# Kernel optimization log

Measured on AMD Instinct MI355X. Metric: run time of the kernel, lower is better.

## Reference

```python
import jax, jax.numpy as jnp
import numpy as np

EMBED = 1024
HEADS = 16
HEAD_DIM = EMBED // HEADS


def setup_inputs() -> dict:
    key = jax.random.key(0)
    ks = jax.random.split(key, 6)
    N, S = 4, 1024
    query = jax.random.normal(ks[0], (N, S, EMBED), dtype=jnp.float32)
    keys = jax.random.normal(ks[1], (N, S, EMBED), dtype=jnp.float32)
    values = jax.random.normal(ks[2], (N, S, EMBED), dtype=jnp.float32)
    mask = jax.random.randint(ks[3], (N, 1, S, S), 0, 2, dtype=jnp.int32)
    W_out = jax.random.normal(ks[4], (EMBED, EMBED), dtype=jnp.float32) * (1.0 / np.sqrt(EMBED))
    b_out = jax.random.normal(ks[5], (EMBED,), dtype=jnp.float32) * 0.02
    return {"query": query, "keys": keys, "values": values, "mask": mask,
            "W_out": W_out, "b_out": b_out}


def reference(query, keys, values, mask, W_out, b_out):
    N, Q, _ = query.shape
    K = keys.shape[1]
    # NOTE: the torch module never applies its per-head q/k/v Linear layers;
    # only the reshape + attention + fc_out are in the forward path.
    q = query.reshape(N, Q, HEADS, HEAD_DIM)
    k = keys.reshape(N, K, HEADS, HEAD_DIM)
    v = values.reshape(N, K, HEADS, HEAD_DIM)
    # energy: [N, H, Q, K]
    energy = jnp.einsum("bqhd,bkhd->bhqk", q, k)
    energy = jnp.where(mask == 0, jnp.float32(-1e20), energy)
    attn = jax.nn.softmax(energy / jnp.sqrt(jnp.float32(HEAD_DIM)), axis=3)
    out = jnp.einsum("bhqk,bkhd->bqhd", attn, v).reshape(N, Q, HEADS * HEAD_DIM)
    return out @ W_out.T + b_out
```

## Files before the change

kernel.cpp:

```cpp
#include <hip/hip_runtime.h>
#include <math.h>

#define NB 4
#define SL 1024
#define EMB 1024
#define NH 16
#define HD 64
#define QB 128

typedef __attribute__((ext_vector_type(8))) short bf16x8;
typedef __attribute__((ext_vector_type(4))) float f32x4;

static __device__ __forceinline__ unsigned pk2(float a, float b) {
    unsigned x = __float_as_uint(a) + 0x8000u;
    unsigned y = __float_as_uint(b) + 0x8000u;
    return (x >> 16) | (y & 0xFFFF0000u);
}
static __device__ __forceinline__ float exp2_fast(float x) {
    float r; asm("v_exp_f32 %0, %1" : "=v"(r) : "v"(x)); return r;
}
static __device__ __forceinline__ void gload_lds16(const void* g, void* l) {
    __builtin_amdgcn_global_load_lds(
        (const __attribute__((address_space(1))) unsigned int*)g,
        (__attribute__((address_space(3))) unsigned int*)l, 16, 0, 0);
}

#define VMW(n) asm volatile("s_waitcnt vmcnt(" #n ")" ::: "memory")
#define MEMPIN() asm volatile("" ::: "memory")

__global__ __launch_bounds__(256) void prep(
    const float* __restrict__ W, unsigned short* __restrict__ Wb,
    const float* __restrict__ Kf, unsigned short* __restrict__ Kb,
    const float* __restrict__ V, unsigned short* __restrict__ Vt,
    const int* __restrict__ mask, unsigned long long* __restrict__ Mbt)
{
    __shared__ unsigned short sT[128 * 68];
    const int bid = blockIdx.x, tid = threadIdx.x;

    if (bid < 512) {
        int i = (bid * 256 + tid) * 8;
        float4 f0 = *(const float4*)&W[i];
        float4 f1 = *(const float4*)&W[i + 4];
        uint4 u = { pk2(f0.x,f0.y), pk2(f0.z,f0.w), pk2(f1.x,f1.y), pk2(f1.z,f1.w) };
        *(uint4*)&Wb[i] = u;
    } else if (bid < 2560) {
        int t = bid - 512;
        int b = t >> 9, h = (t >> 5) & 15, k0 = (t & 31) * 32;
        int r = tid >> 3, d = (tid & 7) * 8;
        const float* gp = &Kf[((size_t)(b * SL + k0 + r)) * EMB + h * HD + d];
        float4 f0 = *(const float4*)gp, f1 = *(const float4*)(gp + 4);
        uint4 u = { pk2(f0.x,f0.y), pk2(f0.z,f0.w), pk2(f1.x,f1.y), pk2(f1.z,f1.w) };
        *(uint4*)&Kb[((size_t)((b * NH + h) * SL + k0 + r)) * HD + d] = u;
    } else if (bid < 3072) {
        int t = bid - 2560;
        int bh = t >> 3, kb = t & 7;
        int b = bh >> 4, h = bh & 15;
        int k0 = kb * 128;
        #pragma unroll
        for (int i = 0; i < 4; ++i) {
            int lin = (i * 256 + tid) * 8;
            int r = lin >> 6, d = lin & 63;
            const float* gp = &V[((size_t)(b * SL + k0 + r)) * EMB + h * HD + d];
            float4 f0 = *(const float4*)gp, f1 = *(const float4*)(gp + 4);
            uint2 u0 = { pk2(f0.x,f0.y), pk2(f0.z,f0.w) };
            uint2 u1 = { pk2(f1.x,f1.y), pk2(f1.z,f1.w) };
            *(uint2*)&sT[r * 68 + d]     = u0;
            *(uint2*)&sT[r * 68 + d + 4] = u1;
        }
        __syncthreads();
        #pragma unroll
        for (int p = 0; p < 4; ++p) {
            int d = p * 16 + (tid >> 4);
            int c = tid & 15;
            unsigned v[4];
            #pragma unroll
            for (int j = 0; j < 4; ++j) {
                unsigned lo = sT[(c * 8 + 2 * j) * 68 + d];
                unsigned hi = sT[(c * 8 + 2 * j + 1) * 68 + d];
                v[j] = lo | (hi << 16);
            }
            uint4 u = { v[0], v[1], v[2], v[3] };
            *(uint4*)&Vt[((size_t)(bh * HD + d)) * SL + k0 + c * 8] = u;
        }
    } else {
        int t = bid - 3072;
        int lane = tid & 63;
        #pragma unroll
        for (int r = 0; r < 4; ++r) {
            int wid = (t * 4 + (tid >> 6)) * 4 + r;
            int c = wid & 15, q = (wid >> 4) & 1023, bb = wid >> 14;
            int mv = mask[((size_t)bb * SL + q) * SL + c * 64 + lane];
            unsigned long long bits = __ballot(mv != 0);
            if (lane == 0) Mbt[((size_t)bb * 16 + c) * SL + q] = bits;
        }
    }
}

__global__ __launch_bounds__(256, 2) void attn_mfma(
    const float* __restrict__ Q, const unsigned short* __restrict__ Kb,
    const unsigned short* __restrict__ Vt,
    const unsigned long long* __restrict__ Mbt,
    unsigned short* __restrict__ Oa)
{
    const int lin = blockIdx.x;
    const int xcd = lin & 7, slot = lin >> 3;
    const int bh = xcd * 8 + (slot >> 3);
    const int q0 = (slot & 7) * QB;
    const int b = bh >> 4, h = bh & 15;
    const int tid = threadIdx.x;
    const int w = tid >> 6, lane = tid & 63;
    const int m16 = lane & 15, quad = lane >> 4;
    const int lr = lane >> 3, lc = lane & 7;
    const int sr0 = tid >> 3;

    __shared__ __align__(16) unsigned short sK[3][64 * 64];
    __shared__ __align__(16) unsigned short sVt[3][64 * 64];
    __shared__ __align__(16) unsigned short sPQ[QB * 72];
    __shared__ uint2 lut[16];

    if (tid < 16) {
        unsigned w0 = ((tid & 1) ? 0xFFFFu : 0u) | ((tid & 2) ? 0xFFFF0000u : 0u);
        unsigned w1 = ((tid & 4) ? 0xFFFFu : 0u) | ((tid & 8) ? 0xFFFF0000u : 0u);
        lut[tid] = make_uint2(w0, w1);
    }

    const size_t vbase = (size_t)(bh * HD) * SL;
    const size_t kbase = (size_t)(bh * SL) * HD;
    const size_t mbase = (size_t)(b * 16) * SL + q0 + w * 32 + m16;

    float4 qf[4][2];
    #pragma unroll
    for (int it = 0; it < 4; ++it) {
        int r = sr0 + it * 32;
        const float* gp = &Q[((size_t)(b * SL + q0 + r)) * EMB + h * HD + lc * 8];
        qf[it][0] = *(const float4*)gp;
        qf[it][1] = *(const float4*)(gp + 4);
    }
    MEMPIN();
    unsigned long long mbA0, mbA1, mbB0, mbB1, mbC0 = 0, mbC1 = 0;
    #pragma unroll
    for (int i = 0; i < 2; ++i) {
        int row = w * 16 + i * 8;
        gload_lds16(&Vt[vbase + (size_t)(row + lr) * SL + (lc ^ lr) * 8], &sVt[0][row * 64]);
        gload_lds16(&Kb[kbase + (size_t)(row + lr) * HD + (lc ^ lr) * 8], &sK[0][row * 64]);
    }
    MEMPIN();
    mbA0 = Mbt[mbase];
    mbA1 = Mbt[mbase + 16];
    MEMPIN();
    #pragma unroll
    for (int i = 0; i < 2; ++i) {
        int row = w * 16 + i * 8;
        gload_lds16(&Vt[vbase + (size_t)(row + lr) * SL + 64 + (lc ^ lr) * 8], &sVt[1][row * 64]);
        gload_lds16(&Kb[kbase + (size_t)(64 + row + lr) * HD + (lc ^ lr) * 8], &sK[1][row * 64]);
    }
    MEMPIN();
    mbB0 = Mbt[mbase + SL];
    mbB1 = Mbt[mbase + SL + 16];
    MEMPIN();
    #pragma unroll
    for (int it = 0; it < 4; ++it) {
        int r = sr0 + it * 32;
        uint4 u = { pk2(qf[it][0].x, qf[it][0].y), pk2(qf[it][0].z, qf[it][0].w),
                    pk2(qf[it][1].x, qf[it][1].y), pk2(qf[it][1].z, qf[it][1].w) };
        *(uint4*)&sPQ[r * 72 + ((lc ^ (r & 7)) * 8)] = u;
    }
    asm volatile("s_waitcnt lgkmcnt(0)" ::: "memory");
    __builtin_amdgcn_s_barrier();
    __builtin_amdgcn_sched_barrier(0);

    bf16x8 bQ[2][2];
    #pragma unroll
    for (int u = 0; u < 2; ++u) {
        int qrow = w * 32 + u * 16 + m16;
        #pragma unroll
        for (int hh = 0; hh < 2; ++hh)
            bQ[u][hh] = *(const bf16x8*)&sPQ[qrow * 72 + (((hh * 4 + quad) ^ (qrow & 7)) * 8)];
    }

    unsigned short* kc = (unsigned short*)sK[0];
    unsigned short* kn = (unsigned short*)sK[1];
    unsigned short* k2 = (unsigned short*)sK[2];
    unsigned short* vc = (unsigned short*)sVt[0];
    unsigned short* vn = (unsigned short*)sVt[1];
    unsigned short* v2 = (unsigned short*)sVt[2];

    f32x4 O[2][4] = {};
    f32x4 lacc[2] = {};
    const float CSC = 0.125f * 1.44269504f;
    const short one_bf = (short)0x3F80;
    const bf16x8 ones = { one_bf, one_bf, one_bf, one_bf, one_bf, one_bf, one_bf, one_bf };

    for (int kt = 0; kt < 16; ++kt) {
        if (kt < 15) { VMW(8); } else { VMW(2); }
        __builtin_amdgcn_s_barrier();
        __builtin_amdgcn_sched_barrier(0);

        if (kt < 14) {
            const int k0n = (kt + 2) * 64;
            #pragma unroll
            for (int i = 0; i < 2; ++i) {
                int row = w * 16 + i * 8;
                gload_lds16(&Vt[vbase + (size_t)(row + lr) * SL + k0n + (lc ^ lr) * 8],
                            &v2[row * 64]);
                gload_lds16(&Kb[kbase + (size_t)(k0n + row + lr) * HD + (lc ^ lr) * 8],
                            &k2[row * 64]);
            }
            MEMPIN();
            mbC0 = Mbt[mbase + (size_t)(kt + 2) * SL];
            mbC1 = Mbt[mbase + (size_t)(kt + 2) * SL + 16];
            MEMPIN();
        }

        f32x4 sc[2][4];
        __builtin_amdgcn_s_setprio(1);
        #pragma unroll
        for (int t = 0; t < 4; ++t) {
            int krow = t * 16 + m16;
            bf16x8 a0 = *(const bf16x8*)&kc[krow * 64 + ((quad ^ (krow & 7)) * 8)];
            bf16x8 a1 = *(const bf16x8*)&kc[krow * 64 + (((4 + quad) ^ (krow & 7)) * 8)];
            f32x4 z = {0.f, 0.f, 0.f, 0.f};
            sc[0][t] = __builtin_amdgcn_mfma_f32_16x16x32_bf16(a0, bQ[0][0], z,        0,0,0);
            sc[0][t] = __builtin_amdgcn_mfma_f32_16x16x32_bf16(a1, bQ[0][1], sc[0][t], 0,0,0);
            sc[1][t] = __builtin_amdgcn_mfma_f32_16x16x32_bf16(a0, bQ[1][0], z,        0,0,0);
            sc[1][t] = __builtin_amdgcn_mfma_f32_16x16x32_bf16(a1, bQ[1][1], sc[1][t], 0,0,0);
        }
        __builtin_amdgcn_s_setprio(0);

        #pragma unroll
        for (int u = 0; u < 2; ++u) {
            unsigned long long mb = u ? mbA1 : mbA0;
            unsigned wlo = (unsigned)mb, whi = (unsigned)(mb >> 32);
            unsigned short* pr = &sPQ[(w * 32 + u * 16 + m16) * 72];
            #pragma unroll
            for (int t = 0; t < 4; ++t) {
                unsigned word = (t < 2) ? wlo : whi;
                unsigned nib = (word >> ((t & 1) * 16 + quad * 4)) & 0xFu;
                uint2 am = lut[nib];
                uint2 pw;
                pw.x = pk2(exp2_fast(sc[u][t][0] * CSC), exp2_fast(sc[u][t][1] * CSC)) & am.x;
                pw.y = pk2(exp2_fast(sc[u][t][2] * CSC), exp2_fast(sc[u][t][3] * CSC)) & am.y;
                *(uint2*)&pr[t * 16 + quad * 4] = pw;
            }
        }
        asm volatile("s_waitcnt lgkmcnt(0)" ::: "memory");

        bf16x8 bP[2][2];
        #pragma unroll
        for (int u = 0; u < 2; ++u)
            #pragma unroll
            for (int hh = 0; hh < 2; ++hh)
                bP[u][hh] = *(const bf16x8*)&sPQ[(w * 32 + u * 16 + m16) * 72 + hh * 32 + quad * 8];

        __builtin_amdgcn_s_setprio(1);
        lacc[0] = __builtin_amdgcn_mfma_f32_16x16x32_bf16(ones, bP[0][0], lacc[0], 0,0,0);
        lacc[0] = __builtin_amdgcn_mfma_f32_16x16x32_bf16(ones, bP[0][1], lacc[0], 0,0,0);
        lacc[1] = __builtin_amdgcn_mfma_f32_16x16x32_bf16(ones, bP[1][0], lacc[1], 0,0,0);
        lacc[1] = __builtin_amdgcn_mfma_f32_16x16x32_bf16(ones, bP[1][1], lacc[1], 0,0,0);

        #pragma unroll
        for (int dt = 0; dt < 4; ++dt) {
            int drow = dt * 16 + m16;
            bf16x8 v0 = *(const bf16x8*)&vc[drow * 64 + ((quad ^ (drow & 7)) * 8)];
            bf16x8 v1 = *(const bf16x8*)&vc[drow * 64 + (((4 + quad) ^ (drow & 7)) * 8)];
            O[0][dt] = __builtin_amdgcn_mfma_f32_16x16x32_bf16(v0, bP[0][0], O[0][dt], 0,0,0);
            O[0][dt] = __builtin_amdgcn_mfma_f32_16x16x32_bf16(v1, bP[0][1], O[0][dt], 0,0,0);
            O[1][dt] = __builtin_amdgcn_mfma_f32_16x16x32_bf16(v0, bP[1][0], O[1][dt], 0,0,0);
            O[1][dt] = __builtin_amdgcn_mfma_f32_16x16x32_bf16(v1, bP[1][1], O[1][dt], 0,0,0);
        }
        __builtin_amdgcn_s_setprio(0);

        unsigned short* tk = kc; kc = kn; kn = k2; k2 = tk;
        unsigned short* tv = vc; vc = vn; vn = v2; v2 = tv;
        mbA0 = mbB0; mbA1 = mbB1; mbB0 = mbC0; mbB1 = mbC1;
    }

    #pragma unroll
    for (int u = 0; u < 2; ++u) {
        float inv = 1.f / lacc[u][0];
        size_t base = ((size_t)(b * SL + q0 + w * 32 + u * 16 + m16)) * EMB + h * HD + quad * 4;
        #pragma unroll
        for (int dt = 0; dt < 4; ++dt) {
            uint2 ow = { pk2(O[u][dt][0] * inv, O[u][dt][1] * inv),
                         pk2(O[u][dt][2] * inv, O[u][dt][3] * inv) };
            *(uint2*)&Oa[base + dt * 16] = ow;
        }
    }
}

__global__ __launch_bounds__(512, 2) void proj_mfma(
    const unsigned short* __restrict__ A, const unsigned short* __restrict__ Wb,
    const float* __restrict__ bias, float* __restrict__ C)
{
    const int n0 = blockIdx.x * 128;
    const int m0 = blockIdx.y * 128;
    const int tid = threadIdx.x;
    const int w = tid >> 6, lane = tid & 63;
    const int m16 = lane & 15, quad = lane >> 4;
    const int lr = lane >> 3, lc = lane & 7;
    const int wm = (w >> 2) * 64, wn = (w & 3) * 32;

    __shared__ __align__(16) unsigned short sA[2][128 * 64];
    __shared__ __align__(16) unsigned short sW[2][128 * 64];

    f32x4 acc[4][2] = {};

    #pragma unroll
    for (int i = 0; i < 2; ++i) {
        int r = w * 16 + i * 8;
        gload_lds16(&A [(size_t)(m0 + r + lr) * EMB + (lc ^ lr) * 8], &sA[0][r * 64]);
        gload_lds16(&Wb[(size_t)(n0 + r + lr) * EMB + (lc ^ lr) * 8], &sW[0][r * 64]);
    }
    __syncthreads();

    for (int it = 0; it < 16; ++it) {
        const int bf = it & 1;
        if (it < 15) {
            int e0 = (it + 1) * 64;
            #pragma unroll
            for (int i = 0; i < 2; ++i) {
                int r = w * 16 + i * 8;
                gload_lds16(&A [(size_t)(m0 + r + lr) * EMB + e0 + (lc ^ lr) * 8], &sA[bf ^ 1][r * 64]);
                gload_lds16(&Wb[(size_t)(n0 + r + lr) * EMB + e0 + (lc ^ lr) * 8], &sW[bf ^ 1][r * 64]);
            }
        }
        #pragma unroll
        for (int hh = 0; hh < 2; ++hh) {
            bf16x8 af[4], bw[2];
            #pragma unroll
            for (int mt = 0; mt < 4; ++mt) {
                int r = wm + mt * 16 + m16;
                af[mt] = *(const bf16x8*)&sA[bf][r * 64 + (((hh * 4 + quad) ^ (r & 7)) * 8)];
            }
            #pragma unroll
            for (int nt = 0; nt < 2; ++nt) {
                int r = wn + nt * 16 + m16;
                bw[nt] = *(const bf16x8*)&sW[bf][r * 64 + (((hh * 4 + quad) ^ (r & 7)) * 8)];
            }
            #pragma unroll
            for (int mt = 0; mt < 4; ++mt)
                #pragma unroll
                for (int nt = 0; nt < 2; ++nt)
                    acc[mt][nt] = __builtin_amdgcn_mfma_f32_16x16x32_bf16(af[mt], bw[nt], acc[mt][nt], 0,0,0);
        }
        __syncthreads();
    }

    #pragma unroll
    for (int nt = 0; nt < 2; ++nt) {
        float bv = bias[n0 + wn + nt * 16 + m16];
        #pragma unroll
        for (int mt = 0; mt < 4; ++mt) {
            size_t row = (size_t)(m0 + wm + mt * 16 + quad * 4);
            #pragma unroll
            for (int rg = 0; rg < 4; ++rg)
                C[(row + rg) * EMB + n0 + wn + nt * 16 + m16] = acc[mt][nt][rg] + bv;
        }
    }
}

extern "C" void kernel_launch(void* const* d_in, const int* in_sizes, int n_in,
                              void* d_out, int out_size, void* d_ws, size_t ws_size,
                              hipStream_t stream) {
    const float* Q    = (const float*)d_in[0];
    const float* K    = (const float*)d_in[1];
    const float* V    = (const float*)d_in[2];
    const int*   mask = (const int*)  d_in[3];
    const float* W    = (const float*)d_in[4];
    const float* bias = (const float*)d_in[5];

    unsigned short* Oa = (unsigned short*)d_ws;
    unsigned short* Wb = Oa + (size_t)NB * SL * EMB;
    unsigned long long* Mbt = (unsigned long long*)(Wb + (size_t)EMB * EMB);
    unsigned short* Vt = (unsigned short*)(Mbt + (size_t)NB * 16 * SL);
    unsigned short* Kb = Vt + (size_t)NB * NH * HD * SL;

    prep<<<7168, 256, 0, stream>>>(W, Wb, K, Kb, V, Vt, mask, Mbt);
    attn_mfma<<<512, 256, 0, stream>>>(Q, Kb, Vt, Mbt, Oa);
    proj_mfma<<<dim3(EMB / 128, (NB * SL) / 128), 512, 0, stream>>>(Oa, Wb, bias, (float*)d_out);
}
```

Measured before the change: 162.6 us.

## Keep softmax P in registers via permlane swaps and pre-convert Q to bf16

The exponentiated scores are no longer written to shared memory and read back as MFMA operands. They are rearranged across lanes with v_permlane32/16 swap instructions, and the mask is applied with per-register bit masks instead of an LDS lookup table. Q conversion to bf16 moves into the prep kernel as extra blocks, so the attention kernel loads bf16 Q fragments straight from global memory without staging through LDS or an initial barrier. This cuts LDS traffic and waits in the inner loop and frees the sPQ buffer, at the cost of more prep work and an extra workspace write and read of Q.

```diff
diff --git a/kernel.cpp b/kernel.cpp
--- a/kernel.cpp
+++ b/kernel.cpp
@@ -10,6 +10,7 @@
 
 typedef __attribute__((ext_vector_type(8))) short bf16x8;
 typedef __attribute__((ext_vector_type(4))) float f32x4;
+typedef __attribute__((ext_vector_type(4))) unsigned u32x4;
 
 static __device__ __forceinline__ unsigned pk2(float a, float b) {
     unsigned x = __float_as_uint(a) + 0x8000u;
@@ -32,7 +33,8 @@
     const float* __restrict__ W, unsigned short* __restrict__ Wb,
     const float* __restrict__ Kf, unsigned short* __restrict__ Kb,
     const float* __restrict__ V, unsigned short* __restrict__ Vt,
-    const int* __restrict__ mask, unsigned long long* __restrict__ Mbt)
+    const int* __restrict__ mask, unsigned long long* __restrict__ Mbt,
+    const float* __restrict__ Qf, unsigned short* __restrict__ Qb)
 {
     __shared__ unsigned short sT[128 * 68];
     const int bid = blockIdx.x, tid = threadIdx.x;
@@ -82,7 +84,7 @@
             uint4 u = { v[0], v[1], v[2], v[3] };
             *(uint4*)&Vt[((size_t)(bh * HD + d)) * SL + k0 + c * 8] = u;
         }
-    } else {
+    } else if (bid < 7168) {
         int t = bid - 3072;
         int lane = tid & 63;
         #pragma unroll
@@ -93,11 +95,19 @@
             unsigned long long bits = __ballot(mv != 0);
             if (lane == 0) Mbt[((size_t)bb * 16 + c) * SL + q] = bits;
         }
+    } else {
+        int t = bid - 7168;
+        int b = t >> 9, h = (t >> 5) & 15, q0 = (t & 31) * 32;
+        int r = tid >> 3, d = (tid & 7) * 8;
+        const float* gp = &Qf[((size_t)(b * SL + q0 + r)) * EMB + h * HD + d];
+        float4 f0 = *(const float4*)gp, f1 = *(const float4*)(gp + 4);
+        uint4 u = { pk2(f0.x,f0.y), pk2(f0.z,f0.w), pk2(f1.x,f1.y), pk2(f1.z,f1.w) };
+        *(uint4*)&Qb[((size_t)((b * NH + h) * SL + q0 + r)) * HD + d] = u;
     }
 }
 
 __global__ __launch_bounds__(256, 2) void attn_mfma(
-    const float* __restrict__ Q, const unsigned short* __restrict__ Kb,
+    const unsigned short* __restrict__ Qb, const unsigned short* __restrict__ Kb,
     const unsigned short* __restrict__ Vt,
     const unsigned long long* __restrict__ Mbt,
     unsigned short* __restrict__ Oa)
@@ -111,31 +121,21 @@
     const int w = tid >> 6, lane = tid & 63;
     const int m16 = lane & 15, quad = lane >> 4;
     const int lr = lane >> 3, lc = lane & 7;
-    const int sr0 = tid >> 3;
 
     __shared__ __align__(16) unsigned short sK[3][64 * 64];
     __shared__ __align__(16) unsigned short sVt[3][64 * 64];
-    __shared__ __align__(16) unsigned short sPQ[QB * 72];
-    __shared__ uint2 lut[16];
-
-    if (tid < 16) {
-        unsigned w0 = ((tid & 1) ? 0xFFFFu : 0u) | ((tid & 2) ? 0xFFFF0000u : 0u);
-        unsigned w1 = ((tid & 4) ? 0xFFFFu : 0u) | ((tid & 8) ? 0xFFFF0000u : 0u);
-        lut[tid] = make_uint2(w0, w1);
-    }
 
     const size_t vbase = (size_t)(bh * HD) * SL;
     const size_t kbase = (size_t)(bh * SL) * HD;
     const size_t mbase = (size_t)(b * 16) * SL + q0 + w * 32 + m16;
-
-    float4 qf[4][2];
-    #pragma unroll
-    for (int it = 0; it < 4; ++it) {
-        int r = sr0 + it * 32;
-        const float* gp = &Q[((size_t)(b * SL + q0 + r)) * EMB + h * HD + lc * 8];
-        qf[it][0] = *(const float4*)gp;
-        qf[it][1] = *(const float4*)(gp + 4);
-    }
+    const size_t qrowb = (size_t)(bh * SL + q0 + w * 32);
+
+    bf16x8 bQ[2][2];
+    #pragma unroll
+    for (int u = 0; u < 2; ++u)
+        #pragma unroll
+        for (int hh = 0; hh < 2; ++hh)
+            bQ[u][hh] = *(const bf16x8*)&Qb[(qrowb + u * 16 + m16) * HD + hh * 32 + quad * 8];
     MEMPIN();
     unsigned long long mbA0, mbA1, mbB0, mbB1, mbC0 = 0, mbC1 = 0;
     #pragma unroll
@@ -158,25 +158,6 @@
     mbB0 = Mbt[mbase + SL];
     mbB1 = Mbt[mbase + SL + 16];
     MEMPIN();
-    #pragma unroll
-    for (int it = 0; it < 4; ++it) {
-        int r = sr0 + it * 32;
-        uint4 u = { pk2(qf[it][0].x, qf[it][0].y), pk2(qf[it][0].z, qf[it][0].w),
-                    pk2(qf[it][1].x, qf[it][1].y), pk2(qf[it][1].z, qf[it][1].w) };
-        *(uint4*)&sPQ[r * 72 + ((lc ^ (r & 7)) * 8)] = u;
-    }
-    asm volatile("s_waitcnt lgkmcnt(0)" ::: "memory");
-    __builtin_amdgcn_s_barrier();
-    __builtin_amdgcn_sched_barrier(0);
-
-    bf16x8 bQ[2][2];
-    #pragma unroll
-    for (int u = 0; u < 2; ++u) {
-        int qrow = w * 32 + u * 16 + m16;
-        #pragma unroll
-        for (int hh = 0; hh < 2; ++hh)
-            bQ[u][hh] = *(const bf16x8*)&sPQ[qrow * 72 + (((hh * 4 + quad) ^ (qrow & 7)) * 8)];
-    }
 
     unsigned short* kc = (unsigned short*)sK[0];
     unsigned short* kn = (unsigned short*)sK[1];
@@ -227,30 +208,44 @@
         }
         __builtin_amdgcn_s_setprio(0);
 
+        bf16x8 bP[2][2];
         #pragma unroll
         for (int u = 0; u < 2; ++u) {
             unsigned long long mb = u ? mbA1 : mbA0;
-            unsigned wlo = (unsigned)mb, whi = (unsigned)(mb >> 32);
-            unsigned short* pr = &sPQ[(w * 32 + u * 16 + m16) * 72];
+            unsigned mlo = (unsigned)mb, mhi = (unsigned)(mb >> 32);
+            unsigned s0 = mlo >> (quad * 8);
+            unsigned s1 = mhi >> (quad * 8);
+            unsigned wt[4][2];
             #pragma unroll
             for (int t = 0; t < 4; ++t) {
-                unsigned word = (t < 2) ? wlo : whi;
-                unsigned nib = (word >> ((t & 1) * 16 + quad * 4)) & 0xFu;
-                uint2 am = lut[nib];
-                uint2 pw;
-                pw.x = pk2(exp2_fast(sc[u][t][0] * CSC), exp2_fast(sc[u][t][1] * CSC)) & am.x;
-                pw.y = pk2(exp2_fast(sc[u][t][2] * CSC), exp2_fast(sc[u][t][3] * CSC)) & am.y;
-                *(uint2*)&pr[t * 16 + quad * 4] = pw;
-            }
-        }
-        asm volatile("s_waitcnt lgkmcnt(0)" ::: "memory");
-
-        bf16x8 bP[2][2];
-        #pragma unroll
-        for (int u = 0; u < 2; ++u)
+                wt[t][0] = pk2(exp2_fast(sc[u][t][0] * CSC), exp2_fast(sc[u][t][1] * CSC));
+                wt[t][1] = pk2(exp2_fast(sc[u][t][2] * CSC), exp2_fast(sc[u][t][3] * CSC));
+            }
+            unsigned g[2][4];
             #pragma unroll
             for (int hh = 0; hh < 2; ++hh)
-                bP[u][hh] = *(const bf16x8*)&sPQ[(w * 32 + u * 16 + m16) * 72 + hh * 32 + quad * 8];
+                #pragma unroll
+                for (int p = 0; p < 2; ++p) {
+                    unsigned A = wt[2 * hh][p], B = wt[2 * hh + 1][p];
+                    asm("v_permlane32_swap_b32 %0, %1" : "+v"(A), "+v"(B));
+                    asm("v_permlane16_swap_b32 %0, %1" : "+v"(A), "+v"(B));
+                    g[hh][p] = A; g[hh][2 + p] = B;
+                }
+            #pragma unroll
+            for (int hh = 0; hh < 2; ++hh) {
+                unsigned sb = hh ? s1 : s0;
+                #pragma unroll
+                for (int j2 = 0; j2 < 4; ++j2) {
+                    unsigned b2 = (sb >> (2 * j2)) & 3u;
+                    unsigned am = ((b2 & 1u) ? 0xFFFFu : 0u) | ((b2 & 2u) ? 0xFFFF0000u : 0u);
+                    g[hh][j2] &= am;
+                }
+            }
+            u32x4 p0 = { g[0][0], g[0][1], g[0][2], g[0][3] };
+            u32x4 p1 = { g[1][0], g[1][1], g[1][2], g[1][3] };
+            bP[u][0] = __builtin_bit_cast(bf16x8, p0);
+            bP[u][1] = __builtin_bit_cast(bf16x8, p1);
+        }
 
         __builtin_amdgcn_s_setprio(1);
         lacc[0] = __builtin_amdgcn_mfma_f32_16x16x32_bf16(ones, bP[0][0], lacc[0], 0,0,0);
@@ -374,8 +369,9 @@
     unsigned long long* Mbt = (unsigned long long*)(Wb + (size_t)EMB * EMB);
     unsigned short* Vt = (unsigned short*)(Mbt + (size_t)NB * 16 * SL);
     unsigned short* Kb = Vt + (size_t)NB * NH * HD * SL;
-
-    prep<<<7168, 256, 0, stream>>>(W, Wb, K, Kb, V, Vt, mask, Mbt);
-    attn_mfma<<<512, 256, 0, stream>>>(Q, Kb, Vt, Mbt, Oa);
+    unsigned short* Qb = Kb + (size_t)NB * NH * SL * HD;
+
+    prep<<<9216, 256, 0, stream>>>(W, Wb, K, Kb, V, Vt, mask, Mbt, Q, Qb);
+    attn_mfma<<<512, 256, 0, stream>>>(Qb, Kb, Vt, Mbt, Oa);
     proj_mfma<<<dim3(EMB / 128, (NB * SL) / 128), 512, 0, stream>>>(Oa, Wb, bias, (float*)d_out);
 }
```

Measured after the change: 167.5 us. +3.0%, slower.
